# Kernel optimization log

Measured on AMD Instinct MI355X. Metric: run time of the kernel, lower is better.

Reference implementation:

```python
import jax, jax.numpy as jnp
import numpy as np

N, E, IN, H1, H2, C = 50000, 800000, 256, 64, 64, 40
NEG_SLOPE = 0.2


def _glorot(key, shape):
    fan_in = shape[0]
    return jax.random.normal(key, shape, jnp.float32) / np.sqrt(fan_in)


def gat_conv(x, W, al, ar, src, dst, act):
    """DGL-style GATConv (no bias, no residual). al/ar: [H, D]."""
    n = x.shape[0]
    H, D = al.shape
    feat = (x @ W).reshape(n, H, D)                      # [N,H,D]
    el = jnp.sum(feat * al, axis=-1)                     # [N,H]
    er = jnp.sum(feat * ar, axis=-1)                     # [N,H]
    e = jax.nn.leaky_relu(el[src] + er[dst], NEG_SLOPE)  # [E,H]
    # edge softmax over incoming edges of each dst node
    emax = jax.ops.segment_max(e, dst, num_segments=n)
    emax = jnp.where(jnp.isfinite(emax), emax, 0.0)      # guard zero-in-degree
    ex = jnp.exp(e - emax[dst])
    den = jax.ops.segment_sum(ex, dst, num_segments=n)
    alpha = ex / jnp.maximum(den[dst], 1e-9)             # [E,H]
    msg = feat[src] * alpha[..., None]                   # [E,H,D]
    rst = jax.ops.segment_sum(msg, dst, num_segments=n)  # [N,H,D]
    return act(rst) if act is not None else rst


def setup_inputs() -> dict:
    key = jax.random.key(0)
    ks = jax.random.split(key, 24)
    x = jax.random.normal(ks[0], (N, IN), jnp.float32)
    src = jax.random.randint(ks[1], (E,), 0, N, jnp.int32)
    dst = jax.random.randint(ks[2], (E,), 0, N, jnp.int32)
    p = {
        # branch 0 (even): GAT(num_layers=2, heads=[4,1,1])
        "W00": _glorot(ks[3], (IN, 4 * H1)),  "a00l": _glorot(ks[4], (4, H1)),  "a00r": _glorot(ks[5], (4, H1)),
        "W01": _glorot(ks[6], (4 * H1, H1)),  "a01l": _glorot(ks[7], (1, H1)),  "a01r": _glorot(ks[8], (1, H1)),
        "W0f": _glorot(ks[9], (H1, C)),       "a0fl": _glorot(ks[10], (1, C)),  "a0fr": _glorot(ks[11], (1, C)),
        # branch 1 (odd): GAT(num_layers=1, heads=[4,1]) encoder + 1-head output conv
        "W10": _glorot(ks[12], (IN, 4 * H2)), "a10l": _glorot(ks[13], (4, H2)), "a10r": _glorot(ks[14], (4, H2)),
        "W1f": _glorot(ks[15], (4 * H2, H1)), "a1fl": _glorot(ks[16], (1, H1)), "a1fr": _glorot(ks[17], (1, H1)),
        "W1o": _glorot(ks[18], (H1, C)),      "a1ol": _glorot(ks[19], (1, C)),  "a1or": _glorot(ks[20], (1, C)),
    }
    return {"x": x, "src": src, "dst": dst, **p}


def reference(x, src, dst,
              W00, a00l, a00r, W01, a01l, a01r, W0f, a0fl, a0fr,
              W10, a10l, a10r, W1f, a1fl, a1fr, W1o, a1ol, a1or):
    elu = jax.nn.elu
    n = x.shape[0]
    # branch 0: stacked GAT, final layer mean over heads, no activation
    h = gat_conv(x, W00, a00l, a00r, src, dst, elu).reshape(n, -1)   # [N,4*H1]
    h = gat_conv(h, W01, a01l, a01r, src, dst, elu).reshape(n, -1)   # [N,H1]
    y0 = gat_conv(h, W0f, a0fl, a0fr, src, dst, None).mean(axis=1)   # [N,C]
    # branch 1: encoder GAT -> emb, then 1-head output conv with elu
    h = gat_conv(x, W10, a10l, a10r, src, dst, elu).reshape(n, -1)   # [N,4*H2]
    emb = gat_conv(h, W1f, a1fl, a1fr, src, dst, None).mean(axis=1)  # [N,H1]
    y1 = gat_conv(emb, W1o, a1ol, a1or, src, dst, elu)[:, 0, :]      # [N,C]
    return jnp.stack([y0, y1], axis=0)                               # [2,N,C]
```

## Files before the change

### kernel.cpp

```cpp
#include <hip/hip_runtime.h>
#include <math.h>

typedef __attribute__((ext_vector_type(8))) short bf16x8;
typedef __attribute__((ext_vector_type(4))) float f32x4;

#define FMAMIX_LO(acc, pk, s) \
    asm("v_fma_mix_f32 %0, %1, %2, %0 op_sel:[0,0,0] op_sel_hi:[1,0,0]" \
        : "+v"(acc) : "v"(pk), "v"(s))
#define FMAMIX_HI(acc, pk, s) \
    asm("v_fma_mix_f32 %0, %1, %2, %0 op_sel:[1,0,0] op_sel_hi:[1,0,0]" \
        : "+v"(acc) : "v"(pk), "v"(s))

__device__ __forceinline__ unsigned short f2bf(float f) {
    unsigned int u = __float_as_uint(f);
    unsigned int r = (u + 0x7FFF + ((u >> 16) & 1)) >> 16;
    return (unsigned short)r;
}
__device__ __forceinline__ float bf2f(unsigned short h) {
    return __uint_as_float((unsigned int)h << 16);
}
__device__ __forceinline__ void split_bf(float x, unsigned short& hi, unsigned short& lo) {
    hi = f2bf(x);
    lo = f2bf(x - bf2f(hi));
}


__global__ void k_hist(const int* __restrict__ dst, int* __restrict__ deg, int e) {
    int t = blockIdx.x * 256 + threadIdx.x;
    if (t < e) atomicAdd(&deg[dst[t]], 1);
}

__global__ void k_scan1(const int* __restrict__ deg, int* __restrict__ tmp,
                        int* __restrict__ bsum, int n) {
    __shared__ int s[1024];
    int t = threadIdx.x;
    int g = blockIdx.x * 1024 + t;
    int v = (g < n) ? deg[g] : 0;
    s[t] = v;
    __syncthreads();
    for (int off = 1; off < 1024; off <<= 1) {
        int u = (t >= off) ? s[t - off] : 0;
        __syncthreads();
        s[t] += u;
        __syncthreads();
    }
    if (g < n) tmp[g] = s[t];
    if (t == 1023) bsum[blockIdx.x] = s[t];
}

__global__ void k_scan2(int* bsum, int nb) {
    int lane = threadIdx.x;
    int orig = (lane < nb) ? bsum[lane] : 0;
    int v = orig;
    #pragma unroll
    for (int off = 1; off < 64; off <<= 1) {
        int u = __shfl_up(v, off);
        if (lane >= off) v += u;
    }
    if (lane < nb) bsum[lane] = v - orig;
}

__global__ void k_scan3(const int* __restrict__ deg, const int* __restrict__ tmp,
                        const int* __restrict__ bsum, int* __restrict__ rowptr,
                        int* __restrict__ cursor, int n) {
    int g = blockIdx.x * 256 + threadIdx.x;
    if (g < n) {
        int incl = tmp[g] + bsum[g >> 10];
        rowptr[g + 1] = incl;
        cursor[g] = incl - deg[g];
        if (g == 0) rowptr[0] = 0;
    }
}

__global__ void k_scatter(const int* __restrict__ src, const int* __restrict__ dst,
                          int* __restrict__ cursor, int* __restrict__ csr, int e) {
    int t = blockIdx.x * 256 + threadIdx.x;
    if (t < e) {
        int d = dst[t];
        int pos = atomicAdd(&cursor[d], 1);
        csr[pos] = src[t];
    }
}


struct WSeg { const float* W; unsigned short* Wh; unsigned short* Wl; int K; int N; int cnt; };
__global__ void k_castw_all(WSeg s0, WSeg s1, WSeg s2, WSeg s3, WSeg s4, WSeg s5) {
    int t = blockIdx.x * 256 + threadIdx.x;
    WSeg sg;
    if      (t < s0.cnt) { sg = s0; }
    else if ((t -= s0.cnt) < s1.cnt) { sg = s1; }
    else if ((t -= s1.cnt) < s2.cnt) { sg = s2; }
    else if ((t -= s2.cnt) < s3.cnt) { sg = s3; }
    else if ((t -= s3.cnt) < s4.cnt) { sg = s4; }
    else if ((t -= s4.cnt) < s5.cnt) { sg = s5; }
    else return;
    int k = t / sg.N, n = t - k * sg.N;
    unsigned short h, l;
    split_bf(sg.W[t], h, l);
    sg.Wh[n * sg.K + k] = h;
    sg.Wl[n * sg.K + k] = l;
}

#define LDP 40

__global__ __launch_bounds__(256) void k_gemm128f(const float* __restrict__ X,
                                                  const unsigned short* __restrict__ B0h,
                                                  const unsigned short* __restrict__ B0l,
                                                  const unsigned short* __restrict__ B1h,
                                                  const unsigned short* __restrict__ B1l,
                                                  _Float16* __restrict__ C,
                                                  int M, int K,
                                                  const float* __restrict__ a0l,
                                                  const float* __restrict__ a0r,
                                                  const float* __restrict__ a1l,
                                                  const float* __restrict__ a1r,
                                                  float* __restrict__ el8,
                                                  float* __restrict__ er8) {
    int Mb = (M + 127) >> 7;
    int nwg = Mb * 2;
    int v = blockIdx.x;
    int bsel = (v >= nwg) ? 1 : 0;
    v -= bsel * nwg;
    int q = nwg >> 3, r = nwg & 7;
    int xcd = v & 7, idx = v >> 3;
    int wg = (xcd < r ? xcd * (q + 1) : r * (q + 1) + (xcd - r) * q) + idx;
    int bx = wg >> 1, by = wg & 1;
    int row0 = bx * 128, col0 = by * 128;
    const unsigned short* Bh = bsel ? B1h : B0h;
    const unsigned short* Bl = bsel ? B1l : B0l;
    const float* alp = bsel ? a1l : a0l;
    const float* arp = bsel ? a1r : a0r;
    _Float16* Cb = C + bsel * 256;

    __shared__ unsigned short Ash[128 * LDP];
    __shared__ unsigned short Asl[128 * LDP];
    __shared__ unsigned short Bsh[128 * LDP];
    __shared__ unsigned short Bsl[128 * LDP];

    int t = threadIdx.x;
    int w = t >> 6, lane = t & 63;
    int wr = w >> 1, wc = w & 1;
    int lrow = lane & 15, kgrp = (lane >> 4) * 8;
    int trow = t >> 1, tcol = (t & 1) * 16;

    f32x4 acc[4][4];
    #pragma unroll
    for (int mt = 0; mt < 4; ++mt)
        #pragma unroll
        for (int nt = 0; nt < 4; ++nt)
            acc[mt][nt] = (f32x4){0.f, 0.f, 0.f, 0.f};

    for (int k0 = 0; k0 < K; k0 += 32) {
        uint4 ah0 = {0u,0u,0u,0u}, ah1 = {0u,0u,0u,0u};
        uint4 av0 = {0u,0u,0u,0u}, av1 = {0u,0u,0u,0u};
        uint4 b0 = {0u,0u,0u,0u}, b1 = {0u,0u,0u,0u};
        uint4 m0 = {0u,0u,0u,0u}, m1 = {0u,0u,0u,0u};
        int gr = row0 + trow;
        if (gr < M) {
            const float* px = X + (size_t)gr * K + k0 + tcol;
            float4 f0 = *(const float4*)px;
            float4 f1 = *(const float4*)(px + 4);
            float4 f2 = *(const float4*)(px + 8);
            float4 f3 = *(const float4*)(px + 12);
            float ff[16] = {f0.x, f0.y, f0.z, f0.w, f1.x, f1.y, f1.z, f1.w,
                            f2.x, f2.y, f2.z, f2.w, f3.x, f3.y, f3.z, f3.w};
            unsigned hp[8], lp[8];
            #pragma unroll
            for (int j = 0; j < 8; ++j) {
                unsigned short ha, la, hb, lb;
                split_bf(ff[2 * j], ha, la);
                split_bf(ff[2 * j + 1], hb, lb);
                hp[j] = (unsigned)ha | ((unsigned)hb << 16);
                lp[j] = (unsigned)la | ((unsigned)lb << 16);
            }
            ah0 = (uint4){hp[0], hp[1], hp[2], hp[3]};
            ah1 = (uint4){hp[4], hp[5], hp[6], hp[7]};
            av0 = (uint4){lp[0], lp[1], lp[2], lp[3]};
            av1 = (uint4){lp[4], lp[5], lp[6], lp[7]};
        }
        int gc = col0 + trow;
        {
            const unsigned short* pb = Bh + (size_t)gc * K + k0 + tcol;
            const unsigned short* pm = Bl + (size_t)gc * K + k0 + tcol;
            b0 = *(const uint4*)pb;       b1 = *(const uint4*)(pb + 8);
            m0 = *(const uint4*)pm;       m1 = *(const uint4*)(pm + 8);
        }
        __syncthreads();
        *(uint4*)&Ash[trow * LDP + tcol]     = ah0;
        *(uint4*)&Ash[trow * LDP + tcol + 8] = ah1;
        *(uint4*)&Asl[trow * LDP + tcol]     = av0;
        *(uint4*)&Asl[trow * LDP + tcol + 8] = av1;
        *(uint4*)&Bsh[trow * LDP + tcol]     = b0;
        *(uint4*)&Bsh[trow * LDP + tcol + 8] = b1;
        *(uint4*)&Bsl[trow * LDP + tcol]     = m0;
        *(uint4*)&Bsl[trow * LDP + tcol + 8] = m1;
        __syncthreads();

        bf16x8 vbh[4], vbl[4];
        #pragma unroll
        for (int nt = 0; nt < 4; ++nt) {
            vbh[nt] = *(const bf16x8*)&Bsh[(wc * 64 + nt * 16 + lrow) * LDP + kgrp];
            vbl[nt] = *(const bf16x8*)&Bsl[(wc * 64 + nt * 16 + lrow) * LDP + kgrp];
        }
        #pragma unroll
        for (int mt = 0; mt < 4; ++mt) {
            bf16x8 vah = *(const bf16x8*)&Ash[(wr * 64 + mt * 16 + lrow) * LDP + kgrp];
            bf16x8 val = *(const bf16x8*)&Asl[(wr * 64 + mt * 16 + lrow) * LDP + kgrp];
            #pragma unroll
            for (int nt = 0; nt < 4; ++nt) {
                acc[mt][nt] = __builtin_amdgcn_mfma_f32_16x16x32_bf16(vah, vbh[nt], acc[mt][nt], 0, 0, 0);
                acc[mt][nt] = __builtin_amdgcn_mfma_f32_16x16x32_bf16(val, vbh[nt], acc[mt][nt], 0, 0, 0);
                acc[mt][nt] = __builtin_amdgcn_mfma_f32_16x16x32_bf16(vah, vbl[nt], acc[mt][nt], 0, 0, 0);
            }
        }
    }

    int orow = (lane >> 4) * 4;
    #pragma unroll
    for (int mt = 0; mt < 4; ++mt) {
        #pragma unroll
        for (int nt = 0; nt < 4; ++nt) {
            int oc = col0 + wc * 64 + nt * 16 + lrow;
            #pragma unroll
            for (int rr = 0; rr < 4; ++rr) {
                int m = row0 + wr * 64 + mt * 16 + orow + rr;
                if (m < M) Cb[(size_t)m * 512 + oc] = (_Float16)acc[mt][nt][rr];
            }
        }
    }

    int h = by * 2 + wc;
    float alv[4], arv[4];
    #pragma unroll
    for (int nt = 0; nt < 4; ++nt) {
        int cidx = nt * 16 + lrow;
        alv[nt] = alp[h * 64 + cidx];
        arv[nt] = arp[h * 64 + cidx];
    }
    #pragma unroll
    for (int mt = 0; mt < 4; ++mt) {
        #pragma unroll
        for (int rr = 0; rr < 4; ++rr) {
            float pl = 0.f, pr = 0.f;
            #pragma unroll
            for (int nt = 0; nt < 4; ++nt) {
                pl = fmaf(acc[mt][nt][rr], alv[nt], pl);
                pr = fmaf(acc[mt][nt][rr], arv[nt], pr);
            }
            #pragma unroll
            for (int off = 1; off < 16; off <<= 1) {
                pl += __shfl_xor(pl, off);
                pr += __shfl_xor(pr, off);
            }
            int m = row0 + wr * 64 + mt * 16 + orow + rr;
            if (lrow == 0 && m < M) {
                el8[m * 8 + h * 2 + bsel] = pl;
                er8[m * 8 + h * 2 + bsel] = pr;
            }
        }
    }
}

__global__ __launch_bounds__(256) void k_gemm_split2(const unsigned short* __restrict__ A0hi,
                                                     const unsigned short* __restrict__ A0lo,
                                                     const unsigned short* __restrict__ B0hp,
                                                     const unsigned short* __restrict__ B0lp,
                                                     const unsigned short* __restrict__ A1hi,
                                                     const unsigned short* __restrict__ A1lo,
                                                     const unsigned short* __restrict__ B1hp,
                                                     const unsigned short* __restrict__ B1lp,
                                                     _Float16* __restrict__ C0,
                                                     _Float16* __restrict__ C1,
                                                     int M, int Ncol, int K, int ldc,
                                                     const float* __restrict__ a0lp,
                                                     const float* __restrict__ a0rp,
                                                     const float* __restrict__ a1lp,
                                                     const float* __restrict__ a1rp,
                                                     float* __restrict__ el2,
                                                     float* __restrict__ er2) {
    int bx = blockIdx.x;
    int bsel = blockIdx.y;
    const unsigned short* Ahi = bsel ? A1hi : A0hi;
    const unsigned short* Alo = bsel ? A1lo : A0lo;
    const unsigned short* Bhi = bsel ? B1hp : B0hp;
    const unsigned short* Blo = bsel ? B1lp : B0lp;
    const float* al = bsel ? a1lp : a0lp;
    const float* ar = bsel ? a1rp : a0rp;
    _Float16* C = bsel ? C1 : C0;

    __shared__ unsigned short Ash[64 * LDP];
    __shared__ unsigned short Asl[64 * LDP];
    __shared__ unsigned short Bsh[64 * LDP];
    __shared__ unsigned short Bsl[64 * LDP];
    int t = threadIdx.x;
    int w = t >> 6, lane = t & 63;
    int lrow = lane & 15, kgrp = (lane >> 4) * 8;
    int row0 = bx * 64;
    int trow = t >> 2, tcol = (t & 3) * 8;

    f32x4 acc[4] = {{0.f, 0.f, 0.f, 0.f}, {0.f, 0.f, 0.f, 0.f},
                    {0.f, 0.f, 0.f, 0.f}, {0.f, 0.f, 0.f, 0.f}};

    for (int k0 = 0; k0 < K; k0 += 32) {
        uint4 ah = {0u,0u,0u,0u}, al4 = {0u,0u,0u,0u};
        uint4 bh = {0u,0u,0u,0u}, bl4 = {0u,0u,0u,0u};
        int gr = row0 + trow;
        if (gr < M) {
            ah  = *(const uint4*)(Ahi + (size_t)gr * K + k0 + tcol);
            al4 = *(const uint4*)(Alo + (size_t)gr * K + k0 + tcol);
        }
        if (trow < Ncol) {
            bh  = *(const uint4*)(Bhi + (size_t)trow * K + k0 + tcol);
            bl4 = *(const uint4*)(Blo + (size_t)trow * K + k0 + tcol);
        }
        __syncthreads();
        *(uint4*)&Ash[trow * LDP + tcol] = ah;
        *(uint4*)&Asl[trow * LDP + tcol] = al4;
        *(uint4*)&Bsh[trow * LDP + tcol] = bh;
        *(uint4*)&Bsl[trow * LDP + tcol] = bl4;
        __syncthreads();
        bf16x8 vbh = *(const bf16x8*)&Bsh[(w * 16 + lrow) * LDP + kgrp];
        bf16x8 vbl = *(const bf16x8*)&Bsl[(w * 16 + lrow) * LDP + kgrp];
        #pragma unroll
        for (int mt = 0; mt < 4; ++mt) {
            bf16x8 vah = *(const bf16x8*)&Ash[(mt * 16 + lrow) * LDP + kgrp];
            bf16x8 val = *(const bf16x8*)&Asl[(mt * 16 + lrow) * LDP + kgrp];
            acc[mt] = __builtin_amdgcn_mfma_f32_16x16x32_bf16(vah, vbh, acc[mt], 0, 0, 0);
            acc[mt] = __builtin_amdgcn_mfma_f32_16x16x32_bf16(val, vbh, acc[mt], 0, 0, 0);
            acc[mt] = __builtin_amdgcn_mfma_f32_16x16x32_bf16(vah, vbl, acc[mt], 0, 0, 0);
        }
    }

    int ocol = w * 16 + lrow;
    int orow = (lane >> 4) * 4;
    if (ocol < Ncol) {
        #pragma unroll
        for (int mt = 0; mt < 4; ++mt) {
            #pragma unroll
            for (int r = 0; r < 4; ++r) {
                int m = row0 + mt * 16 + orow + r;
                if (m < M) C[(size_t)m * ldc + ocol] = (_Float16)acc[mt][r];
            }
        }
    }

    float alv = (ocol < Ncol) ? al[ocol] : 0.f;
    float arv = (ocol < Ncol) ? ar[ocol] : 0.f;
    __syncthreads();
    float* Pl = (float*)Ash;
    float* Pr = (float*)Bsh;
    #pragma unroll
    for (int mt = 0; mt < 4; ++mt) {
        #pragma unroll
        for (int r = 0; r < 4; ++r) {
            float pl = acc[mt][r] * alv;
            float pr = acc[mt][r] * arv;
            #pragma unroll
            for (int off = 1; off < 16; off <<= 1) {
                pl += __shfl_xor(pl, off);
                pr += __shfl_xor(pr, off);
            }
            if (lrow == 0) {
                int rloc = mt * 16 + orow + r;
                Pl[w * 64 + rloc] = pl;
                Pr[w * 64 + rloc] = pr;
            }
        }
    }
    __syncthreads();
    if (t < 64) {
        int m = row0 + t;
        if (m < M) {
            float pl = Pl[t] + Pl[64 + t] + Pl[128 + t] + Pl[192 + t];
            float pr = Pr[t] + Pr[64 + t] + Pr[128 + t] + Pr[192 + t];
            el2[m * 2 + bsel] = pl;
            er2[m * 2 + bsel] = pr;
        }
    }
}

__device__ __forceinline__ float lrelu(float v) { return v > 0.f ? v : 0.2f * v; }

#define A42_ISSUE(J) uint4 q##J = *(const uint4*)(featLane + ((size_t)(unsigned)__shfl(s, (J) << 2) << 10))
#define A42_CONS(J, X) \
    FMAMIX_LO(f0, q##J.x, X); FMAMIX_HI(f1, q##J.x, X); \
    FMAMIX_LO(f2, q##J.y, X); FMAMIX_HI(f3, q##J.y, X); \
    FMAMIX_LO(f4, q##J.z, X); FMAMIX_HI(f5, q##J.z, X); \
    FMAMIX_LO(f6, q##J.w, X); FMAMIX_HI(f7, q##J.w, X)

__global__ __launch_bounds__(256) void k_agg4x2(const int* __restrict__ rowptr,
                                                const int* __restrict__ csr,
                                                const float* __restrict__ el8,
                                                const float* __restrict__ er8,
                                                const _Float16* __restrict__ featC,
                                                unsigned short* __restrict__ b0hi,
                                                unsigned short* __restrict__ b0lo,
                                                unsigned short* __restrict__ b1hi,
                                                unsigned short* __restrict__ b1lo,
                                                int n) {
    __shared__ float s_ex[4][128];
    int w = threadIdx.x >> 6;
    int lane = threadIdx.x & 63;
    int i = blockIdx.x * 4 + w;
    if (i >= n) return;
    int s0 = rowptr[i], s1 = rowptr[i + 1];
    int deg = s1 - s0;
    int eidx = lane >> 2, h = lane & 3;
    int b = lane >> 5, hh = (lane >> 3) & 3;
    float2 erp = *(const float2*)&er8[i * 8 + h * 2];
    const char* featLane = (const char*)featC + (lane << 4);

    float den0 = 0.f, den1 = 0.f;
    float m0 = -INFINITY, m1 = -INFINITY;
    float f0 = 0.f, f1 = 0.f, f2 = 0.f, f3 = 0.f;
    float f4 = 0.f, f5 = 0.f, f6 = 0.f, f7 = 0.f;

    int e0 = s0 + eidx;
    int s = (e0 < s1) ? csr[e0] : 0;
    for (int c = s0; c < s1; c += 16) {
        bool val = (c + eidx < s1);
        float2 elp = *(const float2*)&el8[(s << 3) + h * 2];
        A42_ISSUE(0);  A42_ISSUE(1);  A42_ISSUE(2);  A42_ISSUE(3);
        A42_ISSUE(4);  A42_ISSUE(5);  A42_ISSUE(6);  A42_ISSUE(7);
        A42_ISSUE(8);  A42_ISSUE(9);  A42_ISSUE(10); A42_ISSUE(11);
        A42_ISSUE(12); A42_ISSUE(13); A42_ISSUE(14); A42_ISSUE(15);
        int en = c + 16 + eidx;
        int sn = (en < s1) ? csr[en] : 0;
        float v0 = val ? lrelu(elp.x + erp.x) : -INFINITY;
        float v1 = val ? lrelu(elp.y + erp.y) : -INFINITY;
        float cm0 = v0, cm1 = v1;
        #pragma unroll
        for (int off = 4; off < 64; off <<= 1) {
            cm0 = fmaxf(cm0, __shfl_xor(cm0, off));
            cm1 = fmaxf(cm1, __shfl_xor(cm1, off));
        }
        float mn0 = fmaxf(m0, cm0), mn1 = fmaxf(m1, cm1);
        float sc0 = __expf(m0 - mn0), sc1 = __expf(m1 - mn1);
        m0 = mn0; m1 = mn1;
        float ex0 = val ? __expf(v0 - mn0) : 0.f;
        float ex1 = val ? __expf(v1 - mn1) : 0.f;
        den0 = den0 * sc0 + ex0;
        den1 = den1 * sc1 + ex1;
        s_ex[w][(h << 4) + eidx] = ex0;
        s_ex[w][64 + (h << 4) + eidx] = ex1;
        float sb0 = __shfl(sc0, hh), sb1 = __shfl(sc1, hh);
        float scl = (lane < 32) ? sb0 : sb1;
        f0 *= scl; f1 *= scl; f2 *= scl; f3 *= scl;
        f4 *= scl; f5 *= scl; f6 *= scl; f7 *= scl;
        const float* exrow = &s_ex[w][(b << 6) + (hh << 4)];
        float4 x0 = *(const float4*)&exrow[0];
        float4 x1 = *(const float4*)&exrow[4];
        float4 x2 = *(const float4*)&exrow[8];
        float4 x3 = *(const float4*)&exrow[12];
        A42_CONS(0, x0.x);  A42_CONS(1, x0.y);  A42_CONS(2, x0.z);  A42_CONS(3, x0.w);
        A42_CONS(4, x1.x);  A42_CONS(5, x1.y);  A42_CONS(6, x1.z);  A42_CONS(7, x1.w);
        A42_CONS(8, x2.x);  A42_CONS(9, x2.y);  A42_CONS(10, x2.z); A42_CONS(11, x2.w);
        A42_CONS(12, x3.x); A42_CONS(13, x3.y); A42_CONS(14, x3.z); A42_CONS(15, x3.w);
        s = sn;
    }

    #pragma unroll
    for (int off = 4; off < 64; off <<= 1) {
        den0 += __shfl_xor(den0, off);
        den1 += __shfl_xor(den1, off);
    }
    float db0 = __shfl(den0, hh), db1 = __shfl(den1, hh);
    float d = fmaxf((lane < 32) ? db0 : db1, 1e-9f);

    float o0 = (deg > 0) ? f0 / d : 0.f;
    float o1 = (deg > 0) ? f1 / d : 0.f;
    float o2 = (deg > 0) ? f2 / d : 0.f;
    float o3 = (deg > 0) ? f3 / d : 0.f;
    float o4 = (deg > 0) ? f4 / d : 0.f;
    float o5 = (deg > 0) ? f5 / d : 0.f;
    float o6 = (deg > 0) ? f6 / d : 0.f;
    float o7 = (deg > 0) ? f7 / d : 0.f;
    o0 = o0 > 0.f ? o0 : (__expf(o0) - 1.f);
    o1 = o1 > 0.f ? o1 : (__expf(o1) - 1.f);
    o2 = o2 > 0.f ? o2 : (__expf(o2) - 1.f);
    o3 = o3 > 0.f ? o3 : (__expf(o3) - 1.f);
    o4 = o4 > 0.f ? o4 : (__expf(o4) - 1.f);
    o5 = o5 > 0.f ? o5 : (__expf(o5) - 1.f);
    o6 = o6 > 0.f ? o6 : (__expf(o6) - 1.f);
    o7 = o7 > 0.f ? o7 : (__expf(o7) - 1.f);

    ushort4 vhA, vlA, vhB, vlB;
    split_bf(o0, vhA.x, vlA.x);
    split_bf(o1, vhA.y, vlA.y);
    split_bf(o2, vhA.z, vlA.z);
    split_bf(o3, vhA.w, vlA.w);
    split_bf(o4, vhB.x, vlB.x);
    split_bf(o5, vhB.y, vlB.y);
    split_bf(o6, vhB.z, vlB.z);
    split_bf(o7, vhB.w, vlB.w);
    size_t base = (size_t)i * 256 + ((lane & 31) << 3);
    if (lane < 32) {
        *(ushort4*)&b0hi[base] = vhA;  *(ushort4*)&b0hi[base + 4] = vhB;
        *(ushort4*)&b0lo[base] = vlA;  *(ushort4*)&b0lo[base + 4] = vlB;
    } else {
        *(ushort4*)&b1hi[base] = vhA;  *(ushort4*)&b1hi[base + 4] = vhB;
        *(ushort4*)&b1lo[base] = vlA;  *(ushort4*)&b1lo[base + 4] = vlB;
    }
}

template <int DB, int ACT0, int ACT1, int SPLITOUT>
__global__ __launch_bounds__(256) void k_agg1x2(const int* __restrict__ rowptr,
                                                const int* __restrict__ csr,
                                                const float* __restrict__ el2,
                                                const float* __restrict__ er2,
                                                const _Float16* __restrict__ featC,
                                                unsigned short* __restrict__ o0hi,
                                                unsigned short* __restrict__ o0lo,
                                                unsigned short* __restrict__ o1hi,
                                                unsigned short* __restrict__ o1lo,
                                                float* __restrict__ ofp0,
                                                float* __restrict__ ofp1, int n) {
    __shared__ int   s_off[4][64];
    __shared__ float s_ex0[4][64];
    __shared__ float s_ex1[4][64];
    int w = threadIdx.x >> 6;
    int i = blockIdx.x * 4 + w;
    int lane = threadIdx.x & 63;
    if (i >= n) return;
    int s0 = rowptr[i], s1 = rowptr[i + 1];
    int deg = s1 - s0;
    float2 erp = *(const float2*)&er2[i * 2];
    bool act = lane < DB;
    int b = (lane >= (DB / 2)) ? 1 : 0;
    int loc = lane - b * (DB / 2);
    const char* featLane = (const char*)featC + lane * 4;
    const int ROWB = 4 * DB;

    float den0 = 0.f, den1 = 0.f, acc0 = 0.f, acc1 = 0.f;
    float m0 = -INFINITY, m1 = -INFINITY;

    auto fma_chunk = [&](int cnt) {
        const float* exr = b ? s_ex1[w] : s_ex0[w];
        int j = 0;
        for (; j + 4 <= cnt; j += 4) {
            int4   oj = *(const int4*)&s_off[w][j];
            float4 xj = *(const float4*)&exr[j];
            unsigned u0 = act ? *(const unsigned*)(featLane + oj.x) : 0u;
            unsigned u1 = act ? *(const unsigned*)(featLane + oj.y) : 0u;
            unsigned u2 = act ? *(const unsigned*)(featLane + oj.z) : 0u;
            unsigned u3 = act ? *(const unsigned*)(featLane + oj.w) : 0u;
            FMAMIX_LO(acc0, u0, xj.x); FMAMIX_HI(acc1, u0, xj.x);
            FMAMIX_LO(acc0, u1, xj.y); FMAMIX_HI(acc1, u1, xj.y);
            FMAMIX_LO(acc0, u2, xj.z); FMAMIX_HI(acc1, u2, xj.z);
            FMAMIX_LO(acc0, u3, xj.w); FMAMIX_HI(acc1, u3, xj.w);
        }
        for (; j < cnt; ++j) {
            unsigned u0 = act ? *(const unsigned*)(featLane + s_off[w][j]) : 0u;
            float x = exr[j];
            FMAMIX_LO(acc0, u0, x); FMAMIX_HI(acc1, u0, x);
        }
    };

    for (int c = s0; c < s1; c += 64) {
        int e = c + lane;
        bool val = e < s1;
        int s = 0;
        float2 elp = {0.f, 0.f};
        if (val) {
            s = csr[e];
            elp = *(const float2*)&el2[s * 2];
        }
        float v0 = val ? lrelu(elp.x + erp.x) : -INFINITY;
        float v1 = val ? lrelu(elp.y + erp.y) : -INFINITY;
        float cm0 = v0, cm1 = v1;
        #pragma unroll
        for (int off = 32; off; off >>= 1) {
            cm0 = fmaxf(cm0, __shfl_xor(cm0, off));
            cm1 = fmaxf(cm1, __shfl_xor(cm1, off));
        }
        float mn0 = fmaxf(m0, cm0), mn1 = fmaxf(m1, cm1);
        float sc0 = __expf(m0 - mn0), sc1 = __expf(m1 - mn1);
        m0 = mn0; m1 = mn1;
        float ex0 = val ? __expf(v0 - mn0) : 0.f;
        float ex1 = val ? __expf(v1 - mn1) : 0.f;
        den0 = den0 * sc0 + ex0;
        den1 = den1 * sc1 + ex1;
        float scl = b ? sc1 : sc0;
        acc0 *= scl; acc1 *= scl;
        s_off[w][lane] = s * ROWB;
        s_ex0[w][lane] = ex0;
        s_ex1[w][lane] = ex1;
        fma_chunk(min(64, s1 - c));
    }
    #pragma unroll
    for (int off = 32; off; off >>= 1) {
        den0 += __shfl_xor(den0, off);
        den1 += __shfl_xor(den1, off);
    }
    float d = fmaxf(b ? den1 : den0, 1e-9f);

    float o0 = (deg > 0) ? acc0 / d : 0.f;
    float o1 = (deg > 0) ? acc1 / d : 0.f;
    int actflag = b ? ACT1 : ACT0;
    if (actflag) {
        o0 = o0 > 0.f ? o0 : (__expf(o0) - 1.f);
        o1 = o1 > 0.f ? o1 : (__expf(o1) - 1.f);
    }
    if (act) {
        if (SPLITOUT) {
            unsigned short h0, l0, h1, l1;
            split_bf(o0, h0, l0);
            split_bf(o1, h1, l1);
            ushort2 vh = {h0, h1}, vl = {l0, l1};
            if (b == 0) {
                *(ushort2*)&o0hi[(size_t)i * DB + 2 * loc] = vh;
                *(ushort2*)&o0lo[(size_t)i * DB + 2 * loc] = vl;
            } else {
                *(ushort2*)&o1hi[(size_t)i * DB + 2 * loc] = vh;
                *(ushort2*)&o1lo[(size_t)i * DB + 2 * loc] = vl;
            }
        } else {
            float2 vo = {o0, o1};
            if (b == 0) *(float2*)&ofp0[(size_t)i * DB + 2 * loc] = vo;
            else        *(float2*)&ofp1[(size_t)i * DB + 2 * loc] = vo;
        }
    }
}


extern "C" void kernel_launch(void* const* d_in, const int* in_sizes, int n_in,
                              void* d_out, int out_size, void* d_ws, size_t ws_size,
                              hipStream_t stream) {
    const float* x    = (const float*)d_in[0];
    const int*   src  = (const int*)d_in[1];
    const int*   dst  = (const int*)d_in[2];
    const float* W00  = (const float*)d_in[3];
    const float* a00l = (const float*)d_in[4];
    const float* a00r = (const float*)d_in[5];
    const float* W01  = (const float*)d_in[6];
    const float* a01l = (const float*)d_in[7];
    const float* a01r = (const float*)d_in[8];
    const float* W0f  = (const float*)d_in[9];
    const float* a0fl = (const float*)d_in[10];
    const float* a0fr = (const float*)d_in[11];
    const float* W10  = (const float*)d_in[12];
    const float* a10l = (const float*)d_in[13];
    const float* a10r = (const float*)d_in[14];
    const float* W1f  = (const float*)d_in[15];
    const float* a1fl = (const float*)d_in[16];
    const float* a1fr = (const float*)d_in[17];
    const float* W1o  = (const float*)d_in[18];
    const float* a1ol = (const float*)d_in[19];
    const float* a1or = (const float*)d_in[20];
    float* out = (float*)d_out;

    const int n = in_sizes[0] / 256;
    const int e = in_sizes[1];
    const int C = 40;

    char* p = (char*)d_ws;
    auto alloc = [&](size_t bytes) -> void* {
        void* r = (void*)p;
        p += (bytes + 255) & ~(size_t)255;
        return r;
    };
    int*   deg     = (int*)alloc((size_t)n * 4);
    int*   tmp     = (int*)alloc((size_t)n * 4);
    int*   bsum    = (int*)alloc(64 * 4);
    int*   rowptr  = (int*)alloc((size_t)(n + 1) * 4);
    int*   cursor  = (int*)alloc((size_t)n * 4);
    int*   csr     = (int*)alloc((size_t)e * 4);
    float* el8     = (float*)alloc((size_t)n * 8 * 4);
    float* er8     = (float*)alloc((size_t)n * 8 * 4);
    _Float16* featC = (_Float16*)alloc((size_t)n * 512 * 2 + 256);
    unsigned short* xhi = (unsigned short*)alloc((size_t)n * 256 * 2);
    unsigned short* xlo = (unsigned short*)alloc((size_t)n * 256 * 2);
    unsigned short* hhi = (unsigned short*)alloc((size_t)n * 256 * 2);
    unsigned short* hlo = (unsigned short*)alloc((size_t)n * 256 * 2);
    unsigned short* W00h = (unsigned short*)alloc(256 * 256 * 2);
    unsigned short* W00l = (unsigned short*)alloc(256 * 256 * 2);
    unsigned short* W01h = (unsigned short*)alloc(256 * 64 * 2);
    unsigned short* W01l = (unsigned short*)alloc(256 * 64 * 2);
    unsigned short* W0fh = (unsigned short*)alloc(64 * 40 * 2);
    unsigned short* W0fl = (unsigned short*)alloc(64 * 40 * 2);
    unsigned short* W10h = (unsigned short*)alloc(256 * 256 * 2);
    unsigned short* W10l = (unsigned short*)alloc(256 * 256 * 2);
    unsigned short* W1fh = (unsigned short*)alloc(256 * 64 * 2);
    unsigned short* W1fl = (unsigned short*)alloc(256 * 64 * 2);
    unsigned short* W1oh = (unsigned short*)alloc(64 * 40 * 2);
    unsigned short* W1ol = (unsigned short*)alloc(64 * 40 * 2);

    hipMemsetAsync(deg, 0, (size_t)n * 4, stream);
    k_hist<<<(e + 255) / 256, 256, 0, stream>>>(dst, deg, e);
    int nb = (n + 1023) / 1024;
    k_scan1<<<nb, 1024, 0, stream>>>(deg, tmp, bsum, n);
    k_scan2<<<1, 64, 0, stream>>>(bsum, nb);
    k_scan3<<<(n + 255) / 256, 256, 0, stream>>>(deg, tmp, bsum, rowptr, cursor, n);
    k_scatter<<<(e + 255) / 256, 256, 0, stream>>>(src, dst, cursor, csr, e);

    {
        WSeg s0 = {W00, W00h, W00l, 256, 256, 256 * 256};
        WSeg s1 = {W10, W10h, W10l, 256, 256, 256 * 256};
        WSeg s2 = {W01, W01h, W01l, 256, 64, 256 * 64};
        WSeg s3 = {W1f, W1fh, W1fl, 256, 64, 256 * 64};
        WSeg s4 = {W0f, W0fh, W0fl, 64, 40, 64 * 40};
        WSeg s5 = {W1o, W1oh, W1ol, 64, 40, 64 * 40};
        int tot = 2 * 65536 + 2 * 16384 + 2 * 2560;
        k_castw_all<<<(tot + 255) / 256, 256, 0, stream>>>(s0, s1, s2, s3, s4, s5);
    }

    int gw1 = (n + 3) / 4;
    int Mb128 = (n + 127) / 128;

    k_gemm128f<<<Mb128 * 2 * 2, 256, 0, stream>>>(x, W00h, W00l, W10h, W10l, featC,
                                                  n, 256, a00l, a00r, a10l, a10r,
                                                  el8, er8);
    k_agg4x2<<<gw1, 256, 0, stream>>>(rowptr, csr, el8, er8, featC, hhi, hlo, xhi, xlo, n);

    {
        dim3 g((n + 63) / 64, 2);
        k_gemm_split2<<<g, 256, 0, stream>>>(hhi, hlo, W01h, W01l,
                                             xhi, xlo, W1fh, W1fl,
                                             featC, featC + 64,
                                             n, 64, 256, 128,
                                             a01l, a01r, a1fl, a1fr, el8, er8);
    }
    k_agg1x2<64, 1, 0, 1><<<gw1, 256, 0, stream>>>(rowptr, csr, el8, er8, featC,
                                                   hhi, hlo, xhi, xlo, nullptr, nullptr, n);

    {
        dim3 g((n + 63) / 64, 2);
        k_gemm_split2<<<g, 256, 0, stream>>>(hhi, hlo, W0fh, W0fl,
                                             xhi, xlo, W1oh, W1ol,
                                             featC, featC + 40,
                                             n, C, 64, 80,
                                             a0fl, a0fr, a1ol, a1or, el8, er8);
    }
    k_agg1x2<40, 0, 1, 0><<<gw1, 256, 0, stream>>>(rowptr, csr, el8, er8, featC,
                                                   nullptr, nullptr, nullptr, nullptr,
                                                   out, out + (size_t)n * C, n);
}
```

Measured before the change: 535.5 us.

## Fuse layer-2 aggregation with final 64x40 projection and merge setup kernels

Fuses the second aggregation with the following small GEMM and attention-logit computation. Each wave now multiplies its aggregated 128-wide row by fp32 W0f/W1o held in LDS and writes fp16 features plus el/er directly. This drops the bf16 hi/lo split writes, one GEMM launch, and the intermediate round trip through global memory. It also folds the weight cast into the histogram kernel and the block-sum scan into scan3, removing launches. The cost is that every block reloads 20KB of weights into LDS, and the final projection now runs in plain fp32 FMA instead of split-bf16 MFMA.

```diff
diff --git a/kernel.cpp b/kernel.cpp
--- a/kernel.cpp
+++ b/kernel.cpp
@@ -25,9 +25,27 @@
 }
 
 
-__global__ void k_hist(const int* __restrict__ dst, int* __restrict__ deg, int e) {
-    int t = blockIdx.x * 256 + threadIdx.x;
-    if (t < e) atomicAdd(&deg[dst[t]], 1);
+struct WSeg { const float* W; unsigned short* Wh; unsigned short* Wl; int K; int N; int cnt; };
+
+__global__ void k_hist_cast(const int* __restrict__ dst, int* __restrict__ deg, int e,
+                            int histBlocks, WSeg s0, WSeg s1, WSeg s2, WSeg s3) {
+    if (blockIdx.x < histBlocks) {
+        int t = blockIdx.x * 256 + threadIdx.x;
+        if (t < e) atomicAdd(&deg[dst[t]], 1);
+    } else {
+        int t = (blockIdx.x - histBlocks) * 256 + threadIdx.x;
+        WSeg sg;
+        if      (t < s0.cnt) { sg = s0; }
+        else if ((t -= s0.cnt) < s1.cnt) { sg = s1; }
+        else if ((t -= s1.cnt) < s2.cnt) { sg = s2; }
+        else if ((t -= s2.cnt) < s3.cnt) { sg = s3; }
+        else return;
+        int k = t / sg.N, n = t - k * sg.N;
+        unsigned short h, l;
+        split_bf(sg.W[t], h, l);
+        sg.Wh[n * sg.K + k] = h;
+        sg.Wl[n * sg.K + k] = l;
+    }
 }
 
 __global__ void k_scan1(const int* __restrict__ deg, int* __restrict__ tmp,
@@ -48,24 +66,25 @@
     if (t == 1023) bsum[blockIdx.x] = s[t];
 }
 
-__global__ void k_scan2(int* bsum, int nb) {
-    int lane = threadIdx.x;
-    int orig = (lane < nb) ? bsum[lane] : 0;
-    int v = orig;
-    #pragma unroll
-    for (int off = 1; off < 64; off <<= 1) {
-        int u = __shfl_up(v, off);
-        if (lane >= off) v += u;
-    }
-    if (lane < nb) bsum[lane] = v - orig;
-}
-
 __global__ void k_scan3(const int* __restrict__ deg, const int* __restrict__ tmp,
                         const int* __restrict__ bsum, int* __restrict__ rowptr,
-                        int* __restrict__ cursor, int n) {
+                        int* __restrict__ cursor, int n, int nb) {
+    __shared__ int pre[64];
+    if (threadIdx.x < 64) {
+        int lane = threadIdx.x;
+        int orig = (lane < nb) ? bsum[lane] : 0;
+        int v = orig;
+        #pragma unroll
+        for (int off = 1; off < 64; off <<= 1) {
+            int u = __shfl_up(v, off);
+            if (lane >= off) v += u;
+        }
+        pre[lane] = v - orig;
+    }
+    __syncthreads();
     int g = blockIdx.x * 256 + threadIdx.x;
     if (g < n) {
-        int incl = tmp[g] + bsum[g >> 10];
+        int incl = tmp[g] + pre[g >> 10];
         rowptr[g + 1] = incl;
         cursor[g] = incl - deg[g];
         if (g == 0) rowptr[0] = 0;
@@ -80,25 +99,6 @@
         int pos = atomicAdd(&cursor[d], 1);
         csr[pos] = src[t];
     }
-}
-
-
-struct WSeg { const float* W; unsigned short* Wh; unsigned short* Wl; int K; int N; int cnt; };
-__global__ void k_castw_all(WSeg s0, WSeg s1, WSeg s2, WSeg s3, WSeg s4, WSeg s5) {
-    int t = blockIdx.x * 256 + threadIdx.x;
-    WSeg sg;
-    if      (t < s0.cnt) { sg = s0; }
-    else if ((t -= s0.cnt) < s1.cnt) { sg = s1; }
-    else if ((t -= s1.cnt) < s2.cnt) { sg = s2; }
-    else if ((t -= s2.cnt) < s3.cnt) { sg = s3; }
-    else if ((t -= s3.cnt) < s4.cnt) { sg = s4; }
-    else if ((t -= s4.cnt) < s5.cnt) { sg = s5; }
-    else return;
-    int k = t / sg.N, n = t - k * sg.N;
-    unsigned short h, l;
-    split_bf(sg.W[t], h, l);
-    sg.Wh[n * sg.K + k] = h;
-    sg.Wl[n * sg.K + k] = l;
 }
 
 #define LDP 40
@@ -503,16 +503,155 @@
     }
 }
 
-template <int DB, int ACT0, int ACT1, int SPLITOUT>
+__global__ __launch_bounds__(256) void k_agg1x2_mid(const int* __restrict__ rowptr,
+                                                    const int* __restrict__ csr,
+                                                    const float* __restrict__ el2,
+                                                    const float* __restrict__ er2,
+                                                    const _Float16* __restrict__ featC,
+                                                    const float* __restrict__ W0,
+                                                    const float* __restrict__ W1,
+                                                    const float* __restrict__ a0l,
+                                                    const float* __restrict__ a0r,
+                                                    const float* __restrict__ a1l,
+                                                    const float* __restrict__ a1r,
+                                                    _Float16* __restrict__ featF,
+                                                    float* __restrict__ elo,
+                                                    float* __restrict__ ero, int n) {
+    __shared__ float s_W0[64 * 40];
+    __shared__ float s_W1[64 * 40];
+    __shared__ int   s_off[4][64];
+    __shared__ float s_ex0[4][64];
+    __shared__ float s_ex1[4][64];
+    __shared__ float s_h[4][128];
+    for (int t = threadIdx.x; t < 64 * 40; t += 256) {
+        s_W0[t] = W0[t];
+        s_W1[t] = W1[t];
+    }
+    __syncthreads();
+
+    int w = threadIdx.x >> 6;
+    int i = blockIdx.x * 4 + w;
+    int lane = threadIdx.x & 63;
+    if (i >= n) return;
+    int s0 = rowptr[i], s1 = rowptr[i + 1];
+    int deg = s1 - s0;
+    float2 erp = *(const float2*)&er2[i * 2];
+    int b = (lane >= 32) ? 1 : 0;
+    int loc = lane - b * 32;
+    const char* featLane = (const char*)featC + lane * 4;
+
+    float den0 = 0.f, den1 = 0.f, acc0 = 0.f, acc1 = 0.f;
+    float m0 = -INFINITY, m1 = -INFINITY;
+
+    auto fma_chunk = [&](int cnt) {
+        const float* exr = b ? s_ex1[w] : s_ex0[w];
+        int j = 0;
+        for (; j + 4 <= cnt; j += 4) {
+            int4   oj = *(const int4*)&s_off[w][j];
+            float4 xj = *(const float4*)&exr[j];
+            unsigned u0 = *(const unsigned*)(featLane + oj.x);
+            unsigned u1 = *(const unsigned*)(featLane + oj.y);
+            unsigned u2 = *(const unsigned*)(featLane + oj.z);
+            unsigned u3 = *(const unsigned*)(featLane + oj.w);
+            FMAMIX_LO(acc0, u0, xj.x); FMAMIX_HI(acc1, u0, xj.x);
+            FMAMIX_LO(acc0, u1, xj.y); FMAMIX_HI(acc1, u1, xj.y);
+            FMAMIX_LO(acc0, u2, xj.z); FMAMIX_HI(acc1, u2, xj.z);
+            FMAMIX_LO(acc0, u3, xj.w); FMAMIX_HI(acc1, u3, xj.w);
+        }
+        for (; j < cnt; ++j) {
+            unsigned u0 = *(const unsigned*)(featLane + s_off[w][j]);
+            float x = exr[j];
+            FMAMIX_LO(acc0, u0, x); FMAMIX_HI(acc1, u0, x);
+        }
+    };
+
+    for (int c = s0; c < s1; c += 64) {
+        int e = c + lane;
+        bool val = e < s1;
+        int s = 0;
+        float2 elp = {0.f, 0.f};
+        if (val) {
+            s = csr[e];
+            elp = *(const float2*)&el2[s * 2];
+        }
+        float v0 = val ? lrelu(elp.x + erp.x) : -INFINITY;
+        float v1 = val ? lrelu(elp.y + erp.y) : -INFINITY;
+        float cm0 = v0, cm1 = v1;
+        #pragma unroll
+        for (int off = 32; off; off >>= 1) {
+            cm0 = fmaxf(cm0, __shfl_xor(cm0, off));
+            cm1 = fmaxf(cm1, __shfl_xor(cm1, off));
+        }
+        float mn0 = fmaxf(m0, cm0), mn1 = fmaxf(m1, cm1);
+        float sc0 = __expf(m0 - mn0), sc1 = __expf(m1 - mn1);
+        m0 = mn0; m1 = mn1;
+        float ex0 = val ? __expf(v0 - mn0) : 0.f;
+        float ex1 = val ? __expf(v1 - mn1) : 0.f;
+        den0 = den0 * sc0 + ex0;
+        den1 = den1 * sc1 + ex1;
+        float scl = b ? sc1 : sc0;
+        acc0 *= scl; acc1 *= scl;
+        s_off[w][lane] = s * 256;
+        s_ex0[w][lane] = ex0;
+        s_ex1[w][lane] = ex1;
+        fma_chunk(min(64, s1 - c));
+    }
+    #pragma unroll
+    for (int off = 32; off; off >>= 1) {
+        den0 += __shfl_xor(den0, off);
+        den1 += __shfl_xor(den1, off);
+    }
+    float d = fmaxf(b ? den1 : den0, 1e-9f);
+
+    float o0 = (deg > 0) ? acc0 / d : 0.f;
+    float o1 = (deg > 0) ? acc1 / d : 0.f;
+    if (b == 0) {
+        o0 = o0 > 0.f ? o0 : (__expf(o0) - 1.f);
+        o1 = o1 > 0.f ? o1 : (__expf(o1) - 1.f);
+    }
+    s_h[w][b * 64 + 2 * loc]     = o0;
+    s_h[w][b * 64 + 2 * loc + 1] = o1;
+
+    bool aj = lane < 40;
+    float out0 = 0.f, out1 = 0.f;
+    if (aj) {
+        const float* h0 = &s_h[w][0];
+        const float* h1 = &s_h[w][64];
+        #pragma unroll 8
+        for (int c = 0; c < 64; ++c) {
+            out0 = fmaf(h0[c], s_W0[c * 40 + lane], out0);
+            out1 = fmaf(h1[c], s_W1[c * 40 + lane], out1);
+        }
+    }
+    float pl0 = aj ? out0 * a0l[lane] : 0.f;
+    float pr0 = aj ? out0 * a0r[lane] : 0.f;
+    float pl1 = aj ? out1 * a1l[lane] : 0.f;
+    float pr1 = aj ? out1 * a1r[lane] : 0.f;
+    #pragma unroll
+    for (int off = 32; off; off >>= 1) {
+        pl0 += __shfl_xor(pl0, off);
+        pr0 += __shfl_xor(pr0, off);
+        pl1 += __shfl_xor(pl1, off);
+        pr1 += __shfl_xor(pr1, off);
+    }
+    if (lane == 0) {
+        elo[i * 2]     = pl0;
+        ero[i * 2]     = pr0;
+        elo[i * 2 + 1] = pl1;
+        ero[i * 2 + 1] = pr1;
+    }
+    if (aj) {
+        featF[(size_t)i * 80 + lane]      = (_Float16)out0;
+        featF[(size_t)i * 80 + 40 + lane] = (_Float16)out1;
+    }
+}
+
+template <int DB, int ACT0, int ACT1>
 __global__ __launch_bounds__(256) void k_agg1x2(const int* __restrict__ rowptr,
                                                 const int* __restrict__ csr,
                                                 const float* __restrict__ el2,
                                                 const float* __restrict__ er2,
                                                 const _Float16* __restrict__ featC,
-                                                unsigned short* __restrict__ o0hi,
-                                                unsigned short* __restrict__ o0lo,
-                                                unsigned short* __restrict__ o1hi,
-                                                unsigned short* __restrict__ o1lo,
                                                 float* __restrict__ ofp0,
                                                 float* __restrict__ ofp1, int n) {
     __shared__ int   s_off[4][64];
@@ -602,23 +741,9 @@
         o1 = o1 > 0.f ? o1 : (__expf(o1) - 1.f);
     }
     if (act) {
-        if (SPLITOUT) {
-            unsigned short h0, l0, h1, l1;
-            split_bf(o0, h0, l0);
-            split_bf(o1, h1, l1);
-            ushort2 vh = {h0, h1}, vl = {l0, l1};
-            if (b == 0) {
-                *(ushort2*)&o0hi[(size_t)i * DB + 2 * loc] = vh;
-                *(ushort2*)&o0lo[(size_t)i * DB + 2 * loc] = vl;
-            } else {
-                *(ushort2*)&o1hi[(size_t)i * DB + 2 * loc] = vh;
-                *(ushort2*)&o1lo[(size_t)i * DB + 2 * loc] = vl;
-            }
-        } else {
-            float2 vo = {o0, o1};
-            if (b == 0) *(float2*)&ofp0[(size_t)i * DB + 2 * loc] = vo;
-            else        *(float2*)&ofp1[(size_t)i * DB + 2 * loc] = vo;
-        }
+        float2 vo = {o0, o1};
+        if (b == 0) *(float2*)&ofp0[(size_t)i * DB + 2 * loc] = vo;
+        else        *(float2*)&ofp1[(size_t)i * DB + 2 * loc] = vo;
     }
 }
 
@@ -668,6 +793,7 @@
     float* el8     = (float*)alloc((size_t)n * 8 * 4);
     float* er8     = (float*)alloc((size_t)n * 8 * 4);
     _Float16* featC = (_Float16*)alloc((size_t)n * 512 * 2 + 256);
+    _Float16* featF = featC + (size_t)n * 128;
     unsigned short* xhi = (unsigned short*)alloc((size_t)n * 256 * 2);
     unsigned short* xlo = (unsigned short*)alloc((size_t)n * 256 * 2);
     unsigned short* hhi = (unsigned short*)alloc((size_t)n * 256 * 2);
@@ -676,33 +802,27 @@
     unsigned short* W00l = (unsigned short*)alloc(256 * 256 * 2);
     unsigned short* W01h = (unsigned short*)alloc(256 * 64 * 2);
     unsigned short* W01l = (unsigned short*)alloc(256 * 64 * 2);
-    unsigned short* W0fh = (unsigned short*)alloc(64 * 40 * 2);
-    unsigned short* W0fl = (unsigned short*)alloc(64 * 40 * 2);
     unsigned short* W10h = (unsigned short*)alloc(256 * 256 * 2);
     unsigned short* W10l = (unsigned short*)alloc(256 * 256 * 2);
     unsigned short* W1fh = (unsigned short*)alloc(256 * 64 * 2);
     unsigned short* W1fl = (unsigned short*)alloc(256 * 64 * 2);
-    unsigned short* W1oh = (unsigned short*)alloc(64 * 40 * 2);
-    unsigned short* W1ol = (unsigned short*)alloc(64 * 40 * 2);
 
     hipMemsetAsync(deg, 0, (size_t)n * 4, stream);
-    k_hist<<<(e + 255) / 256, 256, 0, stream>>>(dst, deg, e);
-    int nb = (n + 1023) / 1024;
-    k_scan1<<<nb, 1024, 0, stream>>>(deg, tmp, bsum, n);
-    k_scan2<<<1, 64, 0, stream>>>(bsum, nb);
-    k_scan3<<<(n + 255) / 256, 256, 0, stream>>>(deg, tmp, bsum, rowptr, cursor, n);
-    k_scatter<<<(e + 255) / 256, 256, 0, stream>>>(src, dst, cursor, csr, e);
-
+    int histBlocks = (e + 255) / 256;
     {
         WSeg s0 = {W00, W00h, W00l, 256, 256, 256 * 256};
         WSeg s1 = {W10, W10h, W10l, 256, 256, 256 * 256};
         WSeg s2 = {W01, W01h, W01l, 256, 64, 256 * 64};
         WSeg s3 = {W1f, W1fh, W1fl, 256, 64, 256 * 64};
-        WSeg s4 = {W0f, W0fh, W0fl, 64, 40, 64 * 40};
-        WSeg s5 = {W1o, W1oh, W1ol, 64, 40, 64 * 40};
-        int tot = 2 * 65536 + 2 * 16384 + 2 * 2560;
-        k_castw_all<<<(tot + 255) / 256, 256, 0, stream>>>(s0, s1, s2, s3, s4, s5);
-    }
+        int castTot = 2 * 65536 + 2 * 16384;
+        int castBlocks = (castTot + 255) / 256;
+        k_hist_cast<<<histBlocks + castBlocks, 256, 0, stream>>>(dst, deg, e, histBlocks,
+                                                                 s0, s1, s2, s3);
+    }
+    int nb = (n + 1023) / 1024;
+    k_scan1<<<nb, 1024, 0, stream>>>(deg, tmp, bsum, n);
+    k_scan3<<<(n + 255) / 256, 256, 0, stream>>>(deg, tmp, bsum, rowptr, cursor, n, nb);
+    k_scatter<<<(e + 255) / 256, 256, 0, stream>>>(src, dst, cursor, csr, e);
 
     int gw1 = (n + 3) / 4;
     int Mb128 = (n + 127) / 128;
@@ -720,18 +840,11 @@
                                              n, 64, 256, 128,
                                              a01l, a01r, a1fl, a1fr, el8, er8);
     }
-    k_agg1x2<64, 1, 0, 1><<<gw1, 256, 0, stream>>>(rowptr, csr, el8, er8, featC,
-                                                   hhi, hlo, xhi, xlo, nullptr, nullptr, n);
-
-    {
-        dim3 g((n + 63) / 64, 2);
-        k_gemm_split2<<<g, 256, 0, stream>>>(hhi, hlo, W0fh, W0fl,
-                                             xhi, xlo, W1oh, W1ol,
-                                             featC, featC + 40,
-                                             n, C, 64, 80,
-                                             a0fl, a0fr, a1ol, a1or, el8, er8);
-    }
-    k_agg1x2<40, 0, 1, 0><<<gw1, 256, 0, stream>>>(rowptr, csr, el8, er8, featC,
-                                                   nullptr, nullptr, nullptr, nullptr,
-                                                   out, out + (size_t)n * C, n);
-}
+    k_agg1x2_mid<<<gw1, 256, 0, stream>>>(rowptr, csr, el8, er8, featC,
+                                          W0f, W1o, a0fl, a0fr, a1ol, a1or,
+                                          featF, el8 + 4 * (size_t)n, er8 + 4 * (size_t)n, n);
+
+    k_agg1x2<40, 0, 1><<<gw1, 256, 0, stream>>>(rowptr, csr,
+                                                el8 + 4 * (size_t)n, er8 + 4 * (size_t)n,
+                                                featF, out, out + (size_t)n * C, n);
+}
```

Result: slower. 566.1 us (+5.7%).
